# Performance work log

Measured on AMD Instinct MI355X. Metric: run time of the kernel, lower is better.

## Reference

```python
import jax, jax.numpy as jnp
import numpy as np

N_E = 8192
DIM = 256
BETA = 0.25


def _l2norm(x, eps=1e-12):
    # matches F.normalize(p=2, dim=-1): x / max(||x||, eps)
    n = jnp.sqrt(jnp.sum(x * x, axis=-1, keepdims=True))
    return x / jnp.maximum(n, eps)


def setup_inputs() -> dict:
    key = jax.random.key(0)
    k1, k2 = jax.random.split(key)
    z = jax.random.normal(k1, (8, 1024, DIM), dtype=jnp.float32)
    embedding_weight = jax.random.normal(k2, (N_E, DIM), dtype=jnp.float32)
    return {"z": z, "embedding_weight": embedding_weight}


def reference(z, embedding_weight):
    z = _l2norm(z)                                   # [B,S,D]
    zf = z.reshape(-1, DIM)                          # [N,D]
    embed_norm = _l2norm(embedding_weight)           # [n_e,D]
    # d = ||z||^2 + ||e||^2 - 2 z.e  -> [N, n_e]
    d = (jnp.sum(zf * zf, axis=1, keepdims=True)
         + jnp.sum(embed_norm * embed_norm, axis=1)
         - 2.0 * jnp.einsum('bd,nd->bn', zf, embed_norm))
    encoding_indices = jnp.argmin(d, axis=1).reshape(z.shape[:-1])  # [B,S]
    z_q = embedding_weight[encoding_indices]          # gather raw codes
    z_q = _l2norm(z_q)                                # [B,S,D]
    loss = (BETA * jnp.mean((jax.lax.stop_gradient(z_q) - z) ** 2)
            + jnp.mean((z_q - jax.lax.stop_gradient(z)) ** 2))
    z_q = z + jax.lax.stop_gradient(z_q - z)          # straight-through
    return z_q, loss, encoding_indices
```

## Files before the change

kernel.cpp:

```cpp
#include <hip/hip_runtime.h>
#include <hip/hip_fp16.h>
#include <cfloat>
#include <math.h>

#define DIM    256
#define N_TOK  8192
#define N_E    8192
#define NSEG   1024
#define MARGIN 0.012f

typedef __attribute__((ext_vector_type(8))) short bf16x8;
typedef __attribute__((ext_vector_type(4))) float f32x4;
typedef __attribute__((ext_vector_type(8))) unsigned short ushort8;

__device__ __forceinline__ unsigned short f2bf(float f) {
    unsigned u = __float_as_uint(f);
    unsigned r = u + 0x7fff + ((u >> 16) & 1);
    return (unsigned short)(r >> 16);
}
__device__ __forceinline__ unsigned fkey(float f) {
    unsigned u = __float_as_uint(f);
    return (u & 0x80000000u) ? ~u : (u | 0x80000000u);
}
__device__ __forceinline__ unsigned short f2h(float f) {
    const __half h = __float2half(f);
    return *(const unsigned short*)&h;
}
__device__ __forceinline__ float h2f(unsigned short u) {
    __half_raw r; r.x = u;
    return __half2float((__half)r);
}

__global__ __launch_bounds__(256) void l2norm_all(const float* __restrict__ z,
                                                  const float* __restrict__ emb,
                                                  float* __restrict__ zn,
                                                  unsigned short* __restrict__ zb,
                                                  float* __restrict__ en,
                                                  unsigned short* __restrict__ esw,
                                                  float* __restrict__ e2) {
    const int lane = threadIdx.x & 63;
    const bool isE = blockIdx.x < (N_E / 4);
    const int row = (isE ? blockIdx.x : blockIdx.x - N_E / 4) * 4 + (threadIdx.x >> 6);
    const float* in = isE ? emb : z;
    float* out = isE ? en : zn;
    const float4 v = *(const float4*)(in + row * DIM + lane * 4);
    float s = v.x * v.x + v.y * v.y + v.z * v.z + v.w * v.w;
#pragma unroll
    for (int off = 1; off < 64; off <<= 1) s += __shfl_xor(s, off, 64);
    const float inv = 1.0f / fmaxf(sqrtf(s), 1e-12f);
    const float4 o = make_float4(v.x * inv, v.y * inv, v.z * inv, v.w * inv);
    *(float4*)(out + row * DIM + lane * 4) = o;
    ushort4 ob; ob.x = f2bf(o.x); ob.y = f2bf(o.y); ob.z = f2bf(o.z); ob.w = f2bf(o.w);
    const int k0 = lane * 4;
    if (isE) {
        const size_t sidx = ((size_t)((row >> 4) * 8 + (k0 >> 5)) * 64
                             + ((k0 >> 3) & 3) * 16 + (row & 15)) * 8 + (k0 & 7);
        *(ushort4*)(esw + sidx) = ob;
        float q = o.x * o.x + o.y * o.y + o.z * o.z + o.w * o.w;
#pragma unroll
        for (int off = 1; off < 64; off <<= 1) q += __shfl_xor(q, off, 64);
        if (lane == 0) e2[row] = q;
    } else {
        *(ushort4*)(zb + (size_t)row * DIM + k0) = ob;
    }
}

__global__ __launch_bounds__(256, 2) void mfma_dist(const unsigned short* __restrict__ zb,
                                                    const unsigned short* __restrict__ esw,
                                                    const float* __restrict__ e2,
                                                    unsigned short* __restrict__ segMh) {
    __shared__ __align__(16) unsigned short As[2][128 * 64];
    float* sm = reinterpret_cast<float*>(As);

    const int tid  = threadIdx.x;
    const int lane = tid & 63;
    const int wave = tid >> 6;
    const int wm = wave & 1, wn = wave >> 1;
    const int row0 = (blockIdx.x & 63) * 128;
    const int col0 = (blockIdx.x >> 6) * 128;
    const int fr = lane & 15, q = lane >> 4;

    f32x4 acc[4][4];
#pragma unroll
    for (int ci = 0; ci < 4; ci++)
#pragma unroll
        for (int zi = 0; zi < 4; zi++) acc[ci][zi] = (f32x4){0.f, 0.f, 0.f, 0.f};

    const int aBase = (col0 >> 4) + wn * 4;
    auto la = [&](int i, int kc) {
        return *(const bf16x8*)(esw + (size_t)(aBase + i) * 4096 + kc * 512 + lane * 8);
    };
    const int cxor = (lane & 7) ^ ((lane >> 3) & 7);
    const unsigned short* gZ = zb + (size_t)(row0 + wave * 32 + (lane >> 3)) * DIM + cxor * 8;
    auto stage = [&](int buf, int p) {
#pragma unroll
        for (int j = 0; j < 4; j++) {
            __builtin_amdgcn_global_load_lds(
                (const __attribute__((address_space(1))) unsigned int*)(gZ + (size_t)j * 8 * DIM + p * 64),
                (__attribute__((address_space(3))) unsigned int*)&As[buf][(wave * 32 + j * 8) * 64],
                16, 0, 0);
        }
    };
    auto lz = [&](int buf, int i, int h) {
        const int r = wm * 64 + i * 16 + fr;
        const int slot = (h * 4 + q) ^ (fr & 7);
        return *(const bf16x8*)&As[buf][r * 64 + slot * 8];
    };

    bf16x8 ca[8][4];
#pragma unroll
    for (int i = 0; i < 4; i++) { ca[0][i] = la(i, 0); ca[1][i] = la(i, 1); }
    stage(0, 0);

#pragma unroll
    for (int p = 0; p < 4; p++) {
        __syncthreads();
        if (p < 3) stage((p + 1) & 1, p + 1);
#pragma unroll
        for (int h = 0; h < 2; h++) {
            const int kc = 2 * p + h;
            if (kc + 2 < 8) {
#pragma unroll
                for (int i = 0; i < 4; i++) ca[kc + 2][i] = la(i, kc + 2);
            }
            bf16x8 zfr[4];
#pragma unroll
            for (int i = 0; i < 4; i++) zfr[i] = lz(p & 1, i, h);
#pragma unroll
            for (int ci = 0; ci < 4; ci++)
#pragma unroll
                for (int zi = 0; zi < 4; zi++)
                    acc[ci][zi] = __builtin_amdgcn_mfma_f32_16x16x32_bf16(ca[kc][ci], zfr[zi], acc[ci][zi], 0, 0, 0);
        }
    }

    float4 e2q[4];
#pragma unroll
    for (int ci = 0; ci < 4; ci++)
        e2q[ci] = *(const float4*)&e2[col0 + wn * 64 + ci * 16 + q * 4];
    __syncthreads();
#pragma unroll
    for (int ci = 0; ci < 4; ci++) {
#pragma unroll
        for (int zi = 0; zi < 4; zi++) {
            const float t0 = fmaf(-2.0f, acc[ci][zi][0], e2q[ci].x);
            const float t1 = fmaf(-2.0f, acc[ci][zi][1], e2q[ci].y);
            const float t2 = fmaf(-2.0f, acc[ci][zi][2], e2q[ci].z);
            const float t3 = fmaf(-2.0f, acc[ci][zi][3], e2q[ci].w);
            float mm = fminf(fminf(t0, t1), fminf(t2, t3));
            mm = fminf(mm, __shfl_xor(mm, 16, 64));
            if (q == 0) sm[(wn * 8 + ci * 2 + 0) * 128 + wm * 64 + zi * 16 + fr] = mm;
            if (q == 2) sm[(wn * 8 + ci * 2 + 1) * 128 + wm * 64 + zi * 16 + fr] = mm;
        }
    }
    __syncthreads();
    {
        const int rl = tid & 127, part = tid >> 7;
        ushort8 o8;
#pragma unroll
        for (int j = 0; j < 8; j++) o8[j] = f2h(sm[(part * 8 + j) * 128 + rl]);
        *(ushort8*)&segMh[(size_t)(row0 + rl) * NSEG + (col0 >> 3) + part * 8] = o8;
    }
}

__global__ __launch_bounds__(256) void select_rescore(const unsigned short* __restrict__ segMh,
                                                      const float* __restrict__ en,
                                                      const float* __restrict__ e2,
                                                      float* zq,
                                                      float* out_base,
                                                      float* __restrict__ pl) {
    const int lane = threadIdx.x & 63;
    const int row  = (blockIdx.x << 2) + (threadIdx.x >> 6);
    const unsigned short* ph = segMh + (size_t)row * NSEG + lane * 16;
    const ushort8 u0 = *(const ushort8*)ph;
    const ushort8 u1 = *(const ushort8*)(ph + 8);
    float vv[16];
#pragma unroll
    for (int j = 0; j < 8; j++) { vv[j] = h2f(u0[j]); vv[8 + j] = h2f(u1[j]); }
    float m = vv[0];
#pragma unroll
    for (int j = 1; j < 16; j++) m = fminf(m, vv[j]);
#pragma unroll
    for (int off = 1; off < 64; off <<= 1) m = fminf(m, __shfl_xor(m, off, 64));
    const float thr = m + MARGIN;

    const int q = lane >> 4, f = lane & 15;
    const float4* zp = (const float4*)(zq + (size_t)row * DIM);
    float4 z4[4];
#pragma unroll
    for (int j = 0; j < 4; j++) z4[j] = zp[j * 16 + f];

    unsigned long long pk = ~0ull;
#pragma unroll
    for (int j = 0; j < 16; j++) {
        unsigned long long bal = __ballot(vv[j] <= thr);
        while (bal) {
            const int l = __ffsll(bal) - 1;
            bal &= bal - 1;
            const int seg = l * 16 + j;
#pragma unroll
            for (int g = 0; g < 2; g++) {
                const int col = seg * 8 + g * 4 + q;
                const float4* ep = (const float4*)(en + (size_t)col * DIM);
                float s = 0.f;
#pragma unroll
                for (int jj = 0; jj < 4; jj++) {
                    const float4 ev = ep[jj * 16 + f];
                    s = fmaf(z4[jj].x, ev.x, s); s = fmaf(z4[jj].y, ev.y, s);
                    s = fmaf(z4[jj].z, ev.z, s); s = fmaf(z4[jj].w, ev.w, s);
                }
#pragma unroll
                for (int off = 1; off < 16; off <<= 1) s += __shfl_xor(s, off, 64);
                const float d = fmaf(-2.0f, s, e2[col]);
                const unsigned long long key =
                    ((unsigned long long)fkey(d) << 32) | (unsigned)col;
                if (key < pk) pk = key;
            }
        }
    }
#pragma unroll
    for (int off = 16; off < 64; off <<= 1) {
        const unsigned long long o = __shfl_xor(pk, off, 64);
        if (o < pk) pk = o;
    }
    const int i = (int)(pk & 0xffffffffu);

    const float4 qv = *(const float4*)(en + (size_t)i * DIM + lane * 4);
    const float4 zv = *(const float4*)(zq + (size_t)row * DIM + lane * 4);
    const float dx = qv.x - zv.x, dy = qv.y - zv.y, dz = qv.z - zv.z, dw = qv.w - zv.w;
    float s = dx * dx + dy * dy + dz * dz + dw * dw;
    *(float4*)(zq + (size_t)row * DIM + lane * 4) = qv;
#pragma unroll
    for (int off = 1; off < 64; off <<= 1) s += __shfl_xor(s, off, 64);
    if (lane == 0) {
        pl[row] = s;
        out_base[N_TOK * DIM + 1 + row] = (float)i;
    }
}

__global__ __launch_bounds__(1024) void finalize_loss(const float* __restrict__ pl,
                                                      float* __restrict__ out) {
    __shared__ float sw[16];
    const int t = threadIdx.x;
    float s = 0.f;
#pragma unroll
    for (int j = 0; j < 8; j++) s += pl[t + j * 1024];
#pragma unroll
    for (int off = 1; off < 64; off <<= 1) s += __shfl_xor(s, off, 64);
    if ((t & 63) == 0) sw[t >> 6] = s;
    __syncthreads();
    if (t < 16) {
        float v = sw[t];
#pragma unroll
        for (int off = 1; off < 16; off <<= 1) v += __shfl_xor(v, off, 64);
        if (t == 0) out[N_TOK * DIM] = v * (1.25f / 2097152.0f);
    }
}

extern "C" void kernel_launch(void* const* d_in, const int* in_sizes, int n_in,
                              void* d_out, int out_size, void* d_ws, size_t ws_size,
                              hipStream_t stream) {
    const float* z   = (const float*)d_in[0];
    const float* emb = (const float*)d_in[1];
    float* out = (float*)d_out;
    char* ws = (char*)d_ws;

    float*          en    = (float*)(ws);
    unsigned short* esw   = (unsigned short*)(ws + 8388608);
    unsigned short* zb    = (unsigned short*)(ws + 12582912);
    float*          e2    = (float*)(ws + 16777216);
    unsigned short* segMh = (unsigned short*)(ws + 16809984);
    float*          pl    = (float*)(ws + 33587200);

    l2norm_all<<<(N_E + N_TOK) / 4, 256, 0, stream>>>(z, emb, out, zb, en, esw, e2);
    mfma_dist<<<64 * 64, 256, 0, stream>>>(zb, esw, e2, segMh);
    select_rescore<<<N_TOK / 4, 256, 0, stream>>>(segMh, en, e2, out, out, pl);
    finalize_loss<<<1, 1024, 0, stream>>>(pl, out);
}
```

Baseline: 137.1 us.

## Split rescore of each token row across four waves via shared candidate list

The select/rescore kernel now assigns one row per 256-thread block instead of one row per wave. The four waves cooperatively find the segment minimum, compact the candidate segments into a shared-memory list with atomics, then split the fp32 rescoring of candidates across waves before a block-level argmin. This is meant to shorten the serial per-row candidate loop and balance uneven candidate counts. The cost is more blocks, extra __syncthreads, and shared-memory atomics.

```diff
diff --git a/kernel.cpp b/kernel.cpp
--- a/kernel.cpp
+++ b/kernel.cpp
@@ -169,53 +169,68 @@
                                                       float* zq,
                                                       float* out_base,
                                                       float* __restrict__ pl) {
-    const int lane = threadIdx.x & 63;
-    const int row  = (blockIdx.x << 2) + (threadIdx.x >> 6);
-    const unsigned short* ph = segMh + (size_t)row * NSEG + lane * 16;
-    const ushort8 u0 = *(const ushort8*)ph;
-    const ushort8 u1 = *(const ushort8*)(ph + 8);
-    float vv[16];
-#pragma unroll
-    for (int j = 0; j < 8; j++) { vv[j] = h2f(u0[j]); vv[8 + j] = h2f(u1[j]); }
-    float m = vv[0];
-#pragma unroll
-    for (int j = 1; j < 16; j++) m = fminf(m, vv[j]);
+    __shared__ float s_wmin[4];
+    __shared__ unsigned long long s_pk[4];
+    __shared__ unsigned short s_list[NSEG];
+    __shared__ int s_cnt;
+
+    const int tid  = threadIdx.x;
+    const int lane = tid & 63;
+    const int wave = tid >> 6;
+    const int row  = blockIdx.x;
+
+    const ushort4 u = *(const ushort4*)(segMh + (size_t)row * NSEG + tid * 4);
+    const float vv[4] = {h2f(u.x), h2f(u.y), h2f(u.z), h2f(u.w)};
+    float m = fminf(fminf(vv[0], vv[1]), fminf(vv[2], vv[3]));
 #pragma unroll
     for (int off = 1; off < 64; off <<= 1) m = fminf(m, __shfl_xor(m, off, 64));
-    const float thr = m + MARGIN;
+    if (lane == 0) s_wmin[wave] = m;
+    if (tid == 0) s_cnt = 0;
+    __syncthreads();
+    const float thr = fminf(fminf(s_wmin[0], s_wmin[1]),
+                            fminf(s_wmin[2], s_wmin[3])) + MARGIN;
+
+#pragma unroll
+    for (int j = 0; j < 4; j++) {
+        const bool fl = vv[j] <= thr;
+        const unsigned long long bal = __ballot(fl);
+        const int cnt = __popcll(bal);
+        int base = 0;
+        if (lane == 0 && cnt) base = atomicAdd(&s_cnt, cnt);
+        base = __shfl(base, 0, 64);
+        if (fl) {
+            const int pos = base + __popcll(bal & ((1ull << lane) - 1));
+            s_list[pos] = (unsigned short)(tid * 4 + j);
+        }
+    }
+    __syncthreads();
+    const int F = s_cnt;
 
     const int q = lane >> 4, f = lane & 15;
     const float4* zp = (const float4*)(zq + (size_t)row * DIM);
     float4 z4[4];
 #pragma unroll
     for (int j = 0; j < 4; j++) z4[j] = zp[j * 16 + f];
-
     unsigned long long pk = ~0ull;
-#pragma unroll
-    for (int j = 0; j < 16; j++) {
-        unsigned long long bal = __ballot(vv[j] <= thr);
-        while (bal) {
-            const int l = __ffsll(bal) - 1;
-            bal &= bal - 1;
-            const int seg = l * 16 + j;
-#pragma unroll
-            for (int g = 0; g < 2; g++) {
-                const int col = seg * 8 + g * 4 + q;
-                const float4* ep = (const float4*)(en + (size_t)col * DIM);
-                float s = 0.f;
-#pragma unroll
-                for (int jj = 0; jj < 4; jj++) {
-                    const float4 ev = ep[jj * 16 + f];
-                    s = fmaf(z4[jj].x, ev.x, s); s = fmaf(z4[jj].y, ev.y, s);
-                    s = fmaf(z4[jj].z, ev.z, s); s = fmaf(z4[jj].w, ev.w, s);
-                }
-#pragma unroll
-                for (int off = 1; off < 16; off <<= 1) s += __shfl_xor(s, off, 64);
-                const float d = fmaf(-2.0f, s, e2[col]);
-                const unsigned long long key =
-                    ((unsigned long long)fkey(d) << 32) | (unsigned)col;
-                if (key < pk) pk = key;
+    for (int e = wave; e < F; e += 4) {
+        const int seg = s_list[e];
+#pragma unroll
+        for (int g = 0; g < 2; g++) {
+            const int col = seg * 8 + g * 4 + q;
+            const float4* ep = (const float4*)(en + (size_t)col * DIM);
+            float s = 0.f;
+#pragma unroll
+            for (int jj = 0; jj < 4; jj++) {
+                const float4 ev = ep[jj * 16 + f];
+                s = fmaf(z4[jj].x, ev.x, s); s = fmaf(z4[jj].y, ev.y, s);
+                s = fmaf(z4[jj].z, ev.z, s); s = fmaf(z4[jj].w, ev.w, s);
             }
+#pragma unroll
+            for (int off = 1; off < 16; off <<= 1) s += __shfl_xor(s, off, 64);
+            const float d = fmaf(-2.0f, s, e2[col]);
+            const unsigned long long key =
+                ((unsigned long long)fkey(d) << 32) | (unsigned)col;
+            if (key < pk) pk = key;
         }
     }
 #pragma unroll
@@ -223,18 +238,30 @@
         const unsigned long long o = __shfl_xor(pk, off, 64);
         if (o < pk) pk = o;
     }
-    const int i = (int)(pk & 0xffffffffu);
-
-    const float4 qv = *(const float4*)(en + (size_t)i * DIM + lane * 4);
-    const float4 zv = *(const float4*)(zq + (size_t)row * DIM + lane * 4);
-    const float dx = qv.x - zv.x, dy = qv.y - zv.y, dz = qv.z - zv.z, dw = qv.w - zv.w;
-    float s = dx * dx + dy * dy + dz * dz + dw * dw;
-    *(float4*)(zq + (size_t)row * DIM + lane * 4) = qv;
-#pragma unroll
-    for (int off = 1; off < 64; off <<= 1) s += __shfl_xor(s, off, 64);
-    if (lane == 0) {
-        pl[row] = s;
-        out_base[N_TOK * DIM + 1 + row] = (float)i;
+    if (lane == 0) s_pk[wave] = pk;
+    __syncthreads();
+
+    if (wave == 0) {
+        unsigned long long p2 = (lane < 4) ? s_pk[lane] : ~0ull;
+#pragma unroll
+        for (int off = 1; off < 4; off <<= 1) {
+            const unsigned long long o = __shfl_xor(p2, off, 64);
+            if (o < p2) p2 = o;
+        }
+        p2 = __shfl(p2, 0, 64);
+        const int i = (int)(p2 & 0xffffffffu);
+        const float4 qv = *(const float4*)(en + (size_t)i * DIM + lane * 4);
+        const float4 zv = *(const float4*)(zq + (size_t)row * DIM + lane * 4);
+        const float dx = qv.x - zv.x, dy = qv.y - zv.y;
+        const float dz = qv.z - zv.z, dw = qv.w - zv.w;
+        float s = dx * dx + dy * dy + dz * dz + dw * dw;
+        *(float4*)(zq + (size_t)row * DIM + lane * 4) = qv;
+#pragma unroll
+        for (int off = 1; off < 64; off <<= 1) s += __shfl_xor(s, off, 64);
+        if (lane == 0) {
+            pl[row] = s;
+            out_base[N_TOK * DIM + 1 + row] = (float)i;
+        }
     }
 }
 
@@ -274,6 +301,6 @@
 
     l2norm_all<<<(N_E + N_TOK) / 4, 256, 0, stream>>>(z, emb, out, zb, en, esw, e2);
     mfma_dist<<<64 * 64, 256, 0, stream>>>(zb, esw, e2, segMh);
-    select_rescore<<<N_TOK / 4, 256, 0, stream>>>(segMh, en, e2, out, out, pl);
+    select_rescore<<<N_TOK, 256, 0, stream>>>(segMh, en, e2, out, out, pl);
     finalize_loss<<<1, 1024, 0, stream>>>(pl, out);
 }
```

Result: slower. 144.3 us (+5.3%).

## Double-buffer candidate codebook loads in rescore and raise mfma_dist occupancy hint

Applied to the files above, without the earlier changes.

The rescore kernel now does a first pass that gathers up to eight candidate segment indices per row into shared memory. A second pass walks that list and prefetches the next candidate's codebook rows and norms into registers while the current candidate is scored, so gather latency overlaps with arithmetic. Candidates beyond eight fall back to the old serial path. Separately, the distance GEMM's launch bound goes from 2 to 3 blocks per CU, which tightens the register budget and may cause spills.

```diff
diff --git a/kernel.cpp b/kernel.cpp
--- a/kernel.cpp
+++ b/kernel.cpp
@@ -65,7 +65,7 @@
     }
 }
 
-__global__ __launch_bounds__(256, 2) void mfma_dist(const unsigned short* __restrict__ zb,
+__global__ __launch_bounds__(256, 3) void mfma_dist(const unsigned short* __restrict__ zb,
                                                     const unsigned short* __restrict__ esw,
                                                     const float* __restrict__ e2,
                                                     unsigned short* __restrict__ segMh) {
@@ -169,8 +169,10 @@
                                                       float* zq,
                                                       float* out_base,
                                                       float* __restrict__ pl) {
+    __shared__ unsigned short s_segs[4][8];
     const int lane = threadIdx.x & 63;
-    const int row  = (blockIdx.x << 2) + (threadIdx.x >> 6);
+    const int wv   = threadIdx.x >> 6;
+    const int row  = (blockIdx.x << 2) + wv;
     const unsigned short* ph = segMh + (size_t)row * NSEG + lane * 16;
     const ushort8 u0 = *(const ushort8*)ph;
     const ushort8 u1 = *(const ushort8*)(ph + 8);
@@ -184,37 +186,85 @@
     for (int off = 1; off < 64; off <<= 1) m = fminf(m, __shfl_xor(m, off, 64));
     const float thr = m + MARGIN;
 
-    const int q = lane >> 4, f = lane & 15;
-    const float4* zp = (const float4*)(zq + (size_t)row * DIM);
-    float4 z4[4];
-#pragma unroll
-    for (int j = 0; j < 4; j++) z4[j] = zp[j * 16 + f];
-
-    unsigned long long pk = ~0ull;
+    int F = 0;
 #pragma unroll
     for (int j = 0; j < 16; j++) {
         unsigned long long bal = __ballot(vv[j] <= thr);
         while (bal) {
             const int l = __ffsll(bal) - 1;
             bal &= bal - 1;
-            const int seg = l * 16 + j;
-#pragma unroll
-            for (int g = 0; g < 2; g++) {
-                const int col = seg * 8 + g * 4 + q;
-                const float4* ep = (const float4*)(en + (size_t)col * DIM);
-                float s = 0.f;
-#pragma unroll
-                for (int jj = 0; jj < 4; jj++) {
-                    const float4 ev = ep[jj * 16 + f];
-                    s = fmaf(z4[jj].x, ev.x, s); s = fmaf(z4[jj].y, ev.y, s);
-                    s = fmaf(z4[jj].z, ev.z, s); s = fmaf(z4[jj].w, ev.w, s);
+            if (F < 8 && lane == 0) s_segs[wv][F] = (unsigned short)(l * 16 + j);
+            F++;
+        }
+    }
+    const int n = (F < 8) ? F : 8;
+
+    const int q = lane >> 4, f = lane & 15;
+    const float4* zp = (const float4*)(zq + (size_t)row * DIM);
+    float4 z4[4];
+#pragma unroll
+    for (int j = 0; j < 4; j++) z4[j] = zp[j * 16 + f];
+
+    unsigned long long pk = ~0ull;
+    auto doload = [&](float4 (&ev)[2][4], float (&ee)[2], int seg) {
+#pragma unroll
+        for (int g = 0; g < 2; g++) {
+            const int col = seg * 8 + g * 4 + q;
+            const float4* ep = (const float4*)(en + (size_t)col * DIM);
+#pragma unroll
+            for (int jj = 0; jj < 4; jj++) ev[g][jj] = ep[jj * 16 + f];
+            ee[g] = e2[col];
+        }
+    };
+    auto dorescore = [&](const float4 (&ev)[2][4], const float (&ee)[2], int seg) {
+#pragma unroll
+        for (int g = 0; g < 2; g++) {
+            float s = 0.f;
+#pragma unroll
+            for (int jj = 0; jj < 4; jj++) {
+                s = fmaf(z4[jj].x, ev[g][jj].x, s); s = fmaf(z4[jj].y, ev[g][jj].y, s);
+                s = fmaf(z4[jj].z, ev[g][jj].z, s); s = fmaf(z4[jj].w, ev[g][jj].w, s);
+            }
+#pragma unroll
+            for (int off = 1; off < 16; off <<= 1) s += __shfl_xor(s, off, 64);
+            const float d = fmaf(-2.0f, s, ee[g]);
+            const int col = seg * 8 + g * 4 + q;
+            const unsigned long long key =
+                ((unsigned long long)fkey(d) << 32) | (unsigned)col;
+            if (key < pk) pk = key;
+        }
+    };
+
+    float4 evA[2][4], evB[2][4];
+    float eA[2], eB[2];
+    int sgA = s_segs[wv][0], sgB = 0;
+    doload(evA, eA, sgA);
+#pragma unroll
+    for (int e = 0; e < 8; e++) {
+        if (e >= n) break;
+        if ((e & 1) == 0) {
+            if (e + 1 < n) { sgB = s_segs[wv][e + 1]; doload(evB, eB, sgB); }
+            dorescore(evA, eA, sgA);
+        } else {
+            if (e + 1 < n) { sgA = s_segs[wv][e + 1]; doload(evA, eA, sgA); }
+            dorescore(evB, eB, sgB);
+        }
+    }
+    if (F > 8) {
+        int c = 0;
+#pragma unroll
+        for (int j = 0; j < 16; j++) {
+            unsigned long long bal = __ballot(vv[j] <= thr);
+            while (bal) {
+                const int l = __ffsll(bal) - 1;
+                bal &= bal - 1;
+                if (c >= 8) {
+                    const int seg = l * 16 + j;
+                    float4 evT[2][4]; float eT[2];
+                    doload(evT, eT, seg);
+                    dorescore(evT, eT, seg);
                 }
-#pragma unroll
-                for (int off = 1; off < 16; off <<= 1) s += __shfl_xor(s, off, 64);
-                const float d = fmaf(-2.0f, s, e2[col]);
-                const unsigned long long key =
-                    ((unsigned long long)fkey(d) << 32) | (unsigned)col;
-                if (key < pk) pk = key;
+                c++;
             }
         }
     }
```

Measured after the change: 139.1 us. No clear change (+1.5%).
